# Optimization experiments

Measured on AMD Instinct MI355X. Metric: run time of the kernel, lower is better.

## Reference

```python
import jax, jax.numpy as jnp
import numpy as np

N_NODES = 100000
N_EDGES = 600000
IN_FEAT = 128
HID = 128
N_CLASSES = 64


def setup_inputs() -> dict:
    key = jax.random.key(0)
    ks = jax.random.split(key, 24)
    inp = {}
    inp["x"] = jax.random.normal(ks[0], (N_NODES, IN_FEAT), dtype=jnp.float32)
    for i, r in enumerate(["r0", "r1"]):
        inp[f"src_{r}"] = jax.random.randint(ks[1 + 3 * i], (N_EDGES,), 0, N_NODES, dtype=jnp.int32)
        inp[f"dst_{r}"] = jax.random.randint(ks[2 + 3 * i], (N_EDGES,), 0, N_NODES, dtype=jnp.int32)
        inp[f"ew_{r}"] = jax.random.uniform(ks[3 + 3 * i], (N_EDGES,), dtype=jnp.float32)
    def glorot(k, shape):
        fan = (shape[0] + shape[1]) / 2.0
        return jax.random.normal(k, shape, dtype=jnp.float32) / jnp.sqrt(fan)
    j = 7
    for r in ["r0", "r1"]:
        inp[f"Ws0_{r}"] = glorot(ks[j], (IN_FEAT, HID)); j += 1
        inp[f"Wn0_{r}"] = glorot(ks[j], (IN_FEAT, HID)); j += 1
        inp[f"b0_{r}"] = jnp.zeros((HID,), jnp.float32)
        inp[f"Wp_{r}"] = glorot(ks[j], (HID, HID)); j += 1
        inp[f"bp_{r}"] = jnp.zeros((HID,), jnp.float32)
        inp[f"Ws1_{r}"] = glorot(ks[j], (HID, N_CLASSES)); j += 1
        inp[f"Wn1_{r}"] = glorot(ks[j], (HID, N_CLASSES)); j += 1
        inp[f"b1_{r}"] = jnp.zeros((N_CLASSES,), jnp.float32)
    return inp


def _mean_agg(feat, src, dst, ew, n_nodes):
    # edge-weighted messages, mean over in-edges (divide by in-degree as DGL does)
    msg = feat[src] * ew[:, None]                      # [E, d]
    s = jax.ops.segment_sum(msg, dst, num_segments=n_nodes)
    deg = jax.ops.segment_sum(jnp.ones_like(ew), dst, num_segments=n_nodes)
    return s / jnp.maximum(deg, 1.0)[:, None]


def _max_agg(feat, src, dst, ew, n_nodes):
    msg = feat[src] * ew[:, None]                      # [E, d]
    m = jax.ops.segment_max(msg, dst, num_segments=n_nodes)
    deg = jax.ops.segment_sum(jnp.ones_like(ew), dst, num_segments=n_nodes)
    return jnp.where(deg[:, None] > 0, m, 0.0)         # zero for isolated nodes


def reference(x, src_r0, dst_r0, ew_r0, src_r1, dst_r1, ew_r1,
              Ws0_r0, Wn0_r0, b0_r0, Ws0_r1, Wn0_r1, b0_r1,
              Wp_r0, bp_r0, Ws1_r0, Wn1_r0, b1_r0,
              Wp_r1, bp_r1, Ws1_r1, Wn1_r1, b1_r1):
    n = x.shape[0]
    # Layer 0: per-relation SAGEConv(mean), HeteroGraphConv aggregate='sum', then relu
    h = jnp.zeros((n, Wn0_r0.shape[1]), x.dtype)
    for src, dst, ew, Ws, Wn, b in [
        (src_r0, dst_r0, ew_r0, Ws0_r0, Wn0_r0, b0_r0),
        (src_r1, dst_r1, ew_r1, Ws0_r1, Wn0_r1, b0_r1),
    ]:
        agg = _mean_agg(x, src, dst, ew, n)
        h = h + x @ Ws + agg @ Wn + b
    h = jax.nn.relu(h)
    # Classifier layer: per-relation SAGEConv(pool): relu(fc_pool(h_src)) -> max-agg
    logits = jnp.zeros((n, Wn1_r0.shape[1]), x.dtype)
    for src, dst, ew, Wp, bp, Ws, Wn, b in [
        (src_r0, dst_r0, ew_r0, Wp_r0, bp_r0, Ws1_r0, Wn1_r0, b1_r0),
        (src_r1, dst_r1, ew_r1, Wp_r1, bp_r1, Ws1_r1, Wn1_r1, b1_r1),
    ]:
        hp = jax.nn.relu(h @ Wp + bp)
        agg = _max_agg(hp, src, dst, ew, n)
        logits = logits + h @ Ws + agg @ Wn + b
    return logits
```

## Files before the change

### kernel.cpp

```cpp
#include <hip/hip_runtime.h>

typedef short bf16x8 __attribute__((ext_vector_type(8)));
typedef float f32x4 __attribute__((ext_vector_type(4)));
typedef float f32x2 __attribute__((ext_vector_type(2)));
typedef unsigned short u16;
typedef unsigned int u32;
typedef unsigned char u8;

#define NN 100000
#define NE 600000
#define PART 12500
#define ECH 4688

__device__ __forceinline__ u16 f2b(float f) {
    u32 u = __float_as_uint(f);
    return (u16)((u + 0x7FFFu + ((u >> 16) & 1u)) >> 16);
}

__global__ __launch_bounds__(256) void deg_part(
    const int* __restrict__ d0, const int* __restrict__ d1,
    int* __restrict__ g0, int* __restrict__ g1)
{
    int part = blockIdx.x & 7;
    int sub = blockIdx.x >> 3;
    int rel = sub & 1;
    int chunk = sub >> 1;
    const int lo = part * PART, hi = lo + PART;
    const int* d = rel ? d1 : d0;
    int* g = rel ? g1 : g0;
    const int e0 = chunk * ECH;
    const int e1 = min(e0 + ECH, NE);
    for (int e = e0 + threadIdx.x; e < e1; e += 256) {
        int dd = d[e];
        if (dd >= lo && dd < hi) atomicAdd(&g[dd], 1);
    }
}

__global__ void fused_setup(
    const float* __restrict__ x, u16* __restrict__ xo, u8* __restrict__ x8,
    const float* __restrict__ Ws0_0, const float* __restrict__ Ws0_1,
    const float* __restrict__ Wn0_0, const float* __restrict__ Wn0_1,
    const float* __restrict__ Wp_0,  const float* __restrict__ Wp_1,
    const float* __restrict__ Ws1_0, const float* __restrict__ Ws1_1,
    const float* __restrict__ Wn1_0, const float* __restrict__ Wn1_1,
    const float* __restrict__ b0_0, const float* __restrict__ b0_1,
    const float* __restrict__ b1_0, const float* __restrict__ b1_1,
    const float* __restrict__ bp_0, const float* __restrict__ bp_1,
    u16* __restrict__ w, float* __restrict__ bsum0, float* __restrict__ bsum1,
    float* __restrict__ bpc)
{
    int bb = blockIdx.x;
    if (bb < 12500) {
        int t = bb * 256 + threadIdx.x;
        const float4 v = reinterpret_cast<const float4*>(x)[t];
        ushort4 r; r.x = f2b(v.x); r.y = f2b(v.y); r.z = f2b(v.z); r.w = f2b(v.w);
        reinterpret_cast<ushort4*>(xo)[t] = r;
        u32 p = __builtin_amdgcn_cvt_pk_fp8_f32(v.x, v.y, 0, false);
        p = __builtin_amdgcn_cvt_pk_fp8_f32(v.z, v.w, p, true);
        reinterpret_cast<u32*>(x8)[t] = p;
    } else {
        int t = (bb - 12500) * 256 + threadIdx.x;
        if (t < 81920) {
            int m = t >> 14, u = t & 16383;
            int n = u >> 7, k = u & 127;
            float v;
            if (m == 0)      v = Ws0_0[k * 128 + n] + Ws0_1[k * 128 + n];
            else if (m == 1) v = Wn0_0[k * 128 + n];
            else if (m == 2) v = Wn0_1[k * 128 + n];
            else if (m == 3) v = Wp_0[k * 128 + n];
            else             v = Wp_1[k * 128 + n];
            w[t] = f2b(v);
        } else if (t < 106496) {
            int u = t - 81920;
            int m = u >> 13; u &= 8191;
            int n = u >> 7, k = u & 127;
            float v;
            if (m == 0)      v = Ws1_0[k * 64 + n] + Ws1_1[k * 64 + n];
            else if (m == 1) v = Wn1_0[k * 64 + n];
            else             v = Wn1_1[k * 64 + n];
            w[t] = f2b(v);
        } else if (t < 106624) {
            int i = t - 106496; bsum0[i] = b0_0[i] + b0_1[i];
        } else if (t < 106688) {
            int i = t - 106624; bsum1[i] = b1_0[i] + b1_1[i];
        } else if (t < 106944) {
            int i = t - 106688; bpc[i] = (i < 128) ? bp_0[i] : bp_1[i - 128];
        }
    }
}

__global__ void scan_local(const int* __restrict__ deg0, const int* __restrict__ deg1,
                           int* __restrict__ offs0, int* __restrict__ offs1,
                           int* __restrict__ bsA, int* __restrict__ bsB)
{
    __shared__ int sm[1024];
    int rel = blockIdx.x >= 98;
    int blk = blockIdx.x - rel * 98;
    const int* in = rel ? deg1 : deg0;
    int* out = rel ? offs1 : offs0;
    int* bsum = rel ? bsB : bsA;
    int t = threadIdx.x;
    int i = blk * 1024 + t;
    int v = (i < NN) ? in[i] : 0;
    sm[t] = v;
    __syncthreads();
    for (int off = 1; off < 1024; off <<= 1) {
        int add = (t >= off) ? sm[t - off] : 0;
        __syncthreads();
        sm[t] += add;
        __syncthreads();
    }
    if (i < NN) out[i] = sm[t] - v;
    if (t == 1023) bsum[blk] = sm[1023];
}

__global__ void scan_bsums(int* __restrict__ bsA, int* __restrict__ bsB)
{
    __shared__ int sm[128];
    int* bsum = blockIdx.x ? bsB : bsA;
    int t = threadIdx.x;
    int v = (t < 98) ? bsum[t] : 0;
    sm[t] = v;
    __syncthreads();
    for (int off = 1; off < 128; off <<= 1) {
        int add = (t >= off) ? sm[t - off] : 0;
        __syncthreads();
        sm[t] += add;
        __syncthreads();
    }
    if (t < 98) bsum[t] = sm[t] - v;
}

__global__ void scan_add(int* __restrict__ offs0, int* __restrict__ offs1,
                         const int* __restrict__ bsA, const int* __restrict__ bsB,
                         int* __restrict__ cur0, int* __restrict__ cur1,
                         u32* __restrict__ csr0, u32* __restrict__ csr1)
{
    int rel = blockIdx.x >= 392;
    int i = (blockIdx.x - rel * 392) * 256 + threadIdx.x;
    int* offs = rel ? offs1 : offs0;
    int* cur = rel ? cur1 : cur0;
    const int* bsum = rel ? bsB : bsA;
    if (i < NN) {
        int v = offs[i] + bsum[i >> 10];
        offs[i] = v;
        cur[i] = v;
    }
    if (i == 0) offs[NN] = NE;
    if (blockIdx.x == 0 && threadIdx.x < 8) {
        csr0[NE + threadIdx.x] = 0;
        csr1[NE + threadIdx.x] = 0;
    }
}

__global__ __launch_bounds__(256) void build_csr_part(
    const int* __restrict__ src0, const int* __restrict__ dst0,
    const float* __restrict__ ew0,
    const int* __restrict__ src1, const int* __restrict__ dst1,
    const float* __restrict__ ew1,
    int* __restrict__ cur0, int* __restrict__ cur1,
    u32* __restrict__ csr0, u32* __restrict__ csr1)
{
    int part = blockIdx.x & 7;
    int sub = blockIdx.x >> 3;
    int rel = sub & 1;
    int chunk = sub >> 1;
    const int lo = part * PART, hi = lo + PART;
    const int* src = rel ? src1 : src0;
    const int* dst = rel ? dst1 : dst0;
    const float* ew = rel ? ew1 : ew0;
    int* cur = rel ? cur1 : cur0;
    u32* csr = rel ? csr1 : csr0;
    const int e0 = chunk * ECH;
    const int e1 = min(e0 + ECH, NE);
    for (int e = e0 + threadIdx.x; e < e1; e += 256) {
        int d = dst[e];
        if (d >= lo && d < hi) {
            int p = atomicAdd(&cur[d], 1);
            u32 q = (__float_as_uint(ew[e]) + 0x10000u) >> 17;
            csr[p] = ((u32)src[e] << 15) | q;
        }
    }
}

template<bool MAXAGG, bool FP8>
__global__ __launch_bounds__(256) void gather(
    const u8* __restrict__ F0, const u8* __restrict__ F1,
    const int* __restrict__ offs0, const u32* __restrict__ csr0, u16* __restrict__ o0,
    const int* __restrict__ offs1, const u32* __restrict__ csr1, u16* __restrict__ o1)
{
    int b = blockIdx.x;
    int rel = b >= 25000;
    const u8* F = rel ? F1 : F0;
    const int* offs = rel ? offs1 : offs0;
    const u32* csr = rel ? csr1 : csr0;
    u16* out = rel ? o1 : o0;
    int node = (b - rel * 25000) * 4 + (threadIdx.x >> 6);
    int lane2 = (threadIdx.x & 63) << 1;
    int beg = __builtin_amdgcn_readfirstlane(offs[node]);
    int end = __builtin_amdgcn_readfirstlane(offs[node + 1]);

    float a0 = 0.f, a1 = 0.f;
    for (int e = beg; e < end; e += 8) {
        u32 E[8], v[8];
#pragma unroll
        for (int i = 0; i < 8; ++i)
            E[i] = csr[e + i];
#pragma unroll
        for (int i = 0; i < 8; ++i) {
            if (FP8)
                v[i] = *reinterpret_cast<const u16*>(F + ((size_t)(E[i] >> 15) << 7) + lane2);
            else
                v[i] = *reinterpret_cast<const u32*>(F + ((size_t)(E[i] >> 15) << 8) + (lane2 << 1));
        }
#pragma unroll
        for (int i = 0; i < 8; ++i) {
            float wgt = (e + i < end) ? __uint_as_float(E[i] << 17) : 0.f;
            float f0, f1;
            if (FP8) {
                f32x2 d = __builtin_amdgcn_cvt_pk_f32_fp8(v[i], false);
                f0 = d.x; f1 = d.y;
            } else {
                f0 = __uint_as_float(v[i] << 16);
                f1 = __uint_as_float(v[i] & 0xFFFF0000u);
            }
            if (MAXAGG) { a0 = fmaxf(a0, f0 * wgt); a1 = fmaxf(a1, f1 * wgt); }
            else        { a0 = fmaf(f0, wgt, a0);   a1 = fmaf(f1, wgt, a1); }
        }
    }
    float s = MAXAGG ? 1.f : 1.f / fmaxf((float)(end - beg), 1.f);
    ushort2 r; r.x = f2b(a0 * s); r.y = f2b(a1 * s);
    *reinterpret_cast<ushort2*>(out + (size_t)node * 128 + lane2) = r;
}

template<int NPAIR, int COLGROUPS, int WAVES, bool RELU, bool OUTF32, bool DUAL>
__global__ __launch_bounds__(WAVES * 64, 2) void gemm_reg(
    const u16* __restrict__ A0, const u16* __restrict__ A1, const u16* __restrict__ A2,
    const u16* __restrict__ BT, const float* __restrict__ bias,
    float* __restrict__ outF, u16* __restrict__ outB, u16* __restrict__ outB2)
{
    constexpr int NC = COLGROUPS * 32;
    constexpr int RT = WAVES / COLGROUPS;
    constexpr int OST = DUAL ? (NC / 2) : NC;
    constexpr int NTILES = NN / 32;
    const int w = threadIdx.x >> 6, l = threadIdx.x & 63;
    const int cg = w % COLGROUPS, rsub = w / COLGROUPS;
    const int l15 = l & 15, lk = (l >> 4) << 3, rq = (l >> 4) << 2;

    bf16x8 bfr[NPAIR][4][2];
#pragma unroll
    for (int p = 0; p < NPAIR; ++p)
#pragma unroll
        for (int ks = 0; ks < 4; ++ks)
#pragma unroll
            for (int cf = 0; cf < 2; ++cf) {
                int n = p * NC + cg * 32 + cf * 16 + l15;
                bfr[p][ks][cf] = *reinterpret_cast<const bf16x8*>(BT + (size_t)n * 128 + ks * 32 + lk);
            }

    const u16* As[3] = {A0, A1, A2};
    const float bv0 = bias[cg * 32 + l15];
    const float bv1 = bias[cg * 32 + 16 + l15];

    for (int tile = blockIdx.x * RT + rsub; tile < NTILES; tile += gridDim.x * RT) {
        const size_t rowbase = (size_t)tile * 32;

        bf16x8 af[NPAIR][4][2];
#pragma unroll
        for (int p = 0; p < NPAIR; ++p) {
            const u16* A = As[p] + rowbase * 128;
#pragma unroll
            for (int ks = 0; ks < 4; ++ks) {
                const int k0 = ks * 32 + lk;
                af[p][ks][0] = *reinterpret_cast<const bf16x8*>(A + (size_t)l15 * 128 + k0);
                af[p][ks][1] = *reinterpret_cast<const bf16x8*>(A + (size_t)(16 + l15) * 128 + k0);
            }
        }

        f32x4 acc[2][2];
#pragma unroll
        for (int rf = 0; rf < 2; ++rf)
#pragma unroll
            for (int cf = 0; cf < 2; ++cf)
                acc[rf][cf] = f32x4{0.f, 0.f, 0.f, 0.f};

#pragma unroll
        for (int p = 0; p < NPAIR; ++p)
#pragma unroll
            for (int ks = 0; ks < 4; ++ks) {
                acc[0][0] = __builtin_amdgcn_mfma_f32_16x16x32_bf16(af[p][ks][0], bfr[p][ks][0], acc[0][0], 0, 0, 0);
                acc[0][1] = __builtin_amdgcn_mfma_f32_16x16x32_bf16(af[p][ks][0], bfr[p][ks][1], acc[0][1], 0, 0, 0);
                acc[1][0] = __builtin_amdgcn_mfma_f32_16x16x32_bf16(af[p][ks][1], bfr[p][ks][0], acc[1][0], 0, 0, 0);
                acc[1][1] = __builtin_amdgcn_mfma_f32_16x16x32_bf16(af[p][ks][1], bfr[p][ks][1], acc[1][1], 0, 0, 0);
            }

        u16* ob = outB;
        if (DUAL && cg >= 4) ob = outB2;
        const int colbase = (DUAL ? (cg & 3) : cg) * 32;
#pragma unroll
        for (int cf = 0; cf < 2; ++cf) {
            const int col = colbase + cf * 16 + l15;
            const float bv = cf ? bv1 : bv0;
#pragma unroll
            for (int rf = 0; rf < 2; ++rf) {
#pragma unroll
                for (int j = 0; j < 4; ++j) {
                    const size_t row = rowbase + rf * 16 + rq + j;
                    float v = acc[rf][cf][j] + bv;
                    if (RELU) v = fmaxf(v, 0.f);
                    if (OUTF32) outF[row * OST + col] = v;
                    else        ob[row * OST + col] = f2b(v);
                }
            }
        }
    }
}

extern "C" void kernel_launch(void* const* d_in, const int* in_sizes, int n_in,
                              void* d_out, int out_size, void* d_ws, size_t ws_size,
                              hipStream_t stream)
{
    const float* x     = (const float*)d_in[0];
    const int*   src0  = (const int*)d_in[1];
    const int*   dst0  = (const int*)d_in[2];
    const float* ew0   = (const float*)d_in[3];
    const int*   src1  = (const int*)d_in[4];
    const int*   dst1  = (const int*)d_in[5];
    const float* ew1   = (const float*)d_in[6];
    const float* Ws0_0 = (const float*)d_in[7];
    const float* Wn0_0 = (const float*)d_in[8];
    const float* b0_0  = (const float*)d_in[9];
    const float* Wp_0  = (const float*)d_in[10];
    const float* bp_0  = (const float*)d_in[11];
    const float* Ws1_0 = (const float*)d_in[12];
    const float* Wn1_0 = (const float*)d_in[13];
    const float* b1_0  = (const float*)d_in[14];
    const float* Ws0_1 = (const float*)d_in[15];
    const float* Wn0_1 = (const float*)d_in[16];
    const float* b0_1  = (const float*)d_in[17];
    const float* Wp_1  = (const float*)d_in[18];
    const float* bp_1  = (const float*)d_in[19];
    const float* Ws1_1 = (const float*)d_in[20];
    const float* Wn1_1 = (const float*)d_in[21];
    const float* b1_1  = (const float*)d_in[22];

    char* ws = (char*)d_ws;
    u16*   x16   = (u16*)(ws + 0);
    u16*   h16   = (u16*)(ws + 25600000);
    u16*   a0    = (u16*)(ws + 51200000);
    u16*   a1    = (u16*)(ws + 76800000);
    u16*   hp1   = (u16*)(ws + 102400000);
    u32*   csr0  = (u32*)(ws + 128000000);
    u32*   csr1  = (u32*)(ws + 130400032);
    int*   offs0 = (int*)(ws + 132800064);
    int*   offs1 = (int*)(ws + 133200080);
    int*   cur0  = (int*)(ws + 133600096);
    int*   cur1  = (int*)(ws + 134000096);
    int*   deg0  = (int*)(ws + 134400096);
    int*   deg1  = (int*)(ws + 134800096);
    int*   bsA   = (int*)(ws + 135200096);
    int*   bsB   = (int*)(ws + 135200608);
    u16*   wts   = (u16*)(ws + 135201120);
    float* bsum0 = (float*)(ws + 135414112);
    float* bsum1 = (float*)(ws + 135414624);
    float* bpc   = (float*)(ws + 135415136);
    u8*    x8    = (u8*)(ws + 136000000);

    u16* hp0 = x16;

    hipMemsetAsync(deg0, 0, 800000, stream);
    deg_part<<<2048, 256, 0, stream>>>(dst0, dst1, deg0, deg1);
    fused_setup<<<12918, 256, 0, stream>>>(
        x, x16, x8, Ws0_0, Ws0_1, Wn0_0, Wn0_1, Wp_0, Wp_1,
        Ws1_0, Ws1_1, Wn1_0, Wn1_1, b0_0, b0_1, b1_0, b1_1, bp_0, bp_1,
        wts, bsum0, bsum1, bpc);

    scan_local<<<196, 1024, 0, stream>>>(deg0, deg1, offs0, offs1, bsA, bsB);
    scan_bsums<<<2, 128, 0, stream>>>(bsA, bsB);
    scan_add<<<784, 256, 0, stream>>>(offs0, offs1, bsA, bsB, cur0, cur1, csr0, csr1);
    build_csr_part<<<2048, 256, 0, stream>>>(
        src0, dst0, ew0, src1, dst1, ew1, cur0, cur1, csr0, csr1);

    gather<false, true><<<50000, 256, 0, stream>>>(
        x8, x8, offs0, csr0, a0, offs1, csr1, a1);
    gemm_reg<3, 4, 4, true, false, false><<<1024, 256, 0, stream>>>(
        x16, a0, a1, wts, bsum0, nullptr, h16, nullptr);

    gemm_reg<1, 8, 8, true, false, true><<<512, 512, 0, stream>>>(
        h16, nullptr, nullptr, wts + 49152, bpc, nullptr, hp0, hp1);
    gather<true, false><<<50000, 256, 0, stream>>>(
        (const u8*)hp0, (const u8*)hp1, offs0, csr0, a0, offs1, csr1, a1);
    gemm_reg<3, 2, 4, false, true, false><<<782, 256, 0, stream>>>(
        h16, a0, a1, wts + 81920, bsum1, (float*)d_out, nullptr, nullptr);
}
```

Measured before the change: 362.3 us.

## Stage A tiles through swizzled double-buffered LDS in first two GEMMs

Adds a gemm_lds kernel that loads each 32-row A tile once into LDS with an XOR swizzle, double-buffers it, and prefetches the next tile into registers while MFMAs run on the current one. It replaces gemm_reg for the layer-0 GEMM and the pool-projection GEMM, with grid sizes changed to 768 persistent blocks. The aim is to stop waves sharing a tile from each re-reading A from global memory and to hide load latency. In exchange it adds LDS usage, a barrier per tile, and drops the occupancy hint from launch_bounds.

```diff
diff --git a/kernel.cpp b/kernel.cpp
--- a/kernel.cpp
+++ b/kernel.cpp
@@ -233,6 +233,129 @@
     *reinterpret_cast<ushort2*>(out + (size_t)node * 128 + lane2) = r;
 }
 
+template<int NPAIR, int COLGROUPS, int WAVES, bool RELU, bool DUAL>
+__global__ __launch_bounds__(WAVES * 64) void gemm_lds(
+    const u16* __restrict__ A0, const u16* __restrict__ A1, const u16* __restrict__ A2,
+    const u16* __restrict__ BT, const float* __restrict__ bias,
+    u16* __restrict__ outB, u16* __restrict__ outB2)
+{
+    constexpr int NC = COLGROUPS * 32;
+    constexpr int OST = DUAL ? (NC / 2) : NC;
+    constexpr int NTILES = NN / 32;
+    constexpr int THREADS = WAVES * 64;
+    constexpr int NLOAD = NPAIR * 512 / THREADS;
+    __shared__ char lds[2 * NPAIR * 8192];
+
+    const int t = threadIdx.x;
+    const int w = t >> 6, l = t & 63;
+    const int cg = w % COLGROUPS;
+    const int l15 = l & 15, lk = (l >> 4) << 3, rq = (l >> 4) << 2;
+
+    const u16* As[3] = {A0, A1, A2};
+
+    int goff[NLOAD], loff[NLOAD];
+#pragma unroll
+    for (int j = 0; j < NLOAD; ++j) {
+        const int p = (j * THREADS) >> 9;
+        const int s = ((j * THREADS) & 511) + t;
+        goff[j] = s * 8;
+        loff[j] = p * 8192 + ((s * 16) ^ (((s >> 4) & 7) << 4));
+    }
+
+    bf16x8 bfr[NPAIR][4][2];
+#pragma unroll
+    for (int p = 0; p < NPAIR; ++p)
+#pragma unroll
+        for (int ks = 0; ks < 4; ++ks)
+#pragma unroll
+            for (int cf = 0; cf < 2; ++cf) {
+                int n = p * NC + cg * 32 + cf * 16 + l15;
+                bfr[p][ks][cf] = *reinterpret_cast<const bf16x8*>(BT + (size_t)n * 128 + ks * 32 + lk);
+            }
+    const float bv0 = bias[cg * 32 + l15];
+    const float bv1 = bias[cg * 32 + 16 + l15];
+
+    u16* ob = outB;
+    if (DUAL && cg >= 4) ob = outB2;
+    const int colbase = (DUAL ? (cg & 3) : cg) * 32;
+
+    uint4 v[NLOAD];
+    int tile = blockIdx.x;
+#pragma unroll
+    for (int j = 0; j < NLOAD; ++j) {
+        const int p = (j * THREADS) >> 9;
+        v[j] = *reinterpret_cast<const uint4*>(As[p] + (size_t)tile * 4096 + goff[j]);
+    }
+#pragma unroll
+    for (int j = 0; j < NLOAD; ++j)
+        *reinterpret_cast<uint4*>(&lds[loff[j]]) = v[j];
+    __syncthreads();
+
+    int buf = 0;
+    while (tile < NTILES) {
+        const int nxt = tile + (int)gridDim.x;
+        if (nxt < NTILES) {
+#pragma unroll
+            for (int j = 0; j < NLOAD; ++j) {
+                const int p = (j * THREADS) >> 9;
+                v[j] = *reinterpret_cast<const uint4*>(As[p] + (size_t)nxt * 4096 + goff[j]);
+            }
+        }
+
+        const int bb = buf * NPAIR * 8192;
+        f32x4 acc[2][2];
+#pragma unroll
+        for (int rf = 0; rf < 2; ++rf)
+#pragma unroll
+            for (int cf = 0; cf < 2; ++cf)
+                acc[rf][cf] = f32x4{0.f, 0.f, 0.f, 0.f};
+        const int sw = (l15 & 7) << 4;
+#pragma unroll
+        for (int p = 0; p < NPAIR; ++p) {
+            const int base = bb + p * 8192;
+#pragma unroll
+            for (int ks = 0; ks < 4; ++ks) {
+                const int cbyte = ks * 64 + lk * 2;
+                bf16x8 a0 = *reinterpret_cast<const bf16x8*>(
+                    &lds[base + ((l15 * 256 + cbyte) ^ sw)]);
+                bf16x8 a1 = *reinterpret_cast<const bf16x8*>(
+                    &lds[base + (((16 + l15) * 256 + cbyte) ^ sw)]);
+                acc[0][0] = __builtin_amdgcn_mfma_f32_16x16x32_bf16(a0, bfr[p][ks][0], acc[0][0], 0, 0, 0);
+                acc[0][1] = __builtin_amdgcn_mfma_f32_16x16x32_bf16(a0, bfr[p][ks][1], acc[0][1], 0, 0, 0);
+                acc[1][0] = __builtin_amdgcn_mfma_f32_16x16x32_bf16(a1, bfr[p][ks][0], acc[1][0], 0, 0, 0);
+                acc[1][1] = __builtin_amdgcn_mfma_f32_16x16x32_bf16(a1, bfr[p][ks][1], acc[1][1], 0, 0, 0);
+            }
+        }
+
+        const size_t rowbase = (size_t)tile * 32;
+#pragma unroll
+        for (int cf = 0; cf < 2; ++cf) {
+            const int col = colbase + cf * 16 + l15;
+            const float bv = cf ? bv1 : bv0;
+#pragma unroll
+            for (int rf = 0; rf < 2; ++rf) {
+#pragma unroll
+                for (int j = 0; j < 4; ++j) {
+                    const size_t row = rowbase + rf * 16 + rq + j;
+                    float vv = acc[rf][cf][j] + bv;
+                    if (RELU) vv = fmaxf(vv, 0.f);
+                    ob[row * OST + col] = f2b(vv);
+                }
+            }
+        }
+
+        if (nxt < NTILES) {
+            const int ob2 = (buf ^ 1) * NPAIR * 8192;
+#pragma unroll
+            for (int j = 0; j < NLOAD; ++j)
+                *reinterpret_cast<uint4*>(&lds[ob2 + loff[j]]) = v[j];
+        }
+        __syncthreads();
+        buf ^= 1;
+        tile = nxt;
+    }
+}
+
 template<int NPAIR, int COLGROUPS, int WAVES, bool RELU, bool OUTF32, bool DUAL>
 __global__ __launch_bounds__(WAVES * 64, 2) void gemm_reg(
     const u16* __restrict__ A0, const u16* __restrict__ A1, const u16* __restrict__ A2,
@@ -383,11 +506,11 @@
 
     gather<false, true><<<50000, 256, 0, stream>>>(
         x8, x8, offs0, csr0, a0, offs1, csr1, a1);
-    gemm_reg<3, 4, 4, true, false, false><<<1024, 256, 0, stream>>>(
-        x16, a0, a1, wts, bsum0, nullptr, h16, nullptr);
-
-    gemm_reg<1, 8, 8, true, false, true><<<512, 512, 0, stream>>>(
-        h16, nullptr, nullptr, wts + 49152, bpc, nullptr, hp0, hp1);
+    gemm_lds<3, 4, 4, true, false><<<768, 256, 0, stream>>>(
+        x16, a0, a1, wts, bsum0, h16, nullptr);
+
+    gemm_lds<1, 8, 8, true, true><<<768, 512, 0, stream>>>(
+        h16, nullptr, nullptr, wts + 49152, bpc, hp0, hp1);
     gather<true, false><<<50000, 256, 0, stream>>>(
         (const u8*)hp0, (const u8*)hp1, offs0, csr0, a0, offs1, csr1, a1);
     gemm_reg<3, 2, 4, false, true, false><<<782, 256, 0, stream>>>(
```

After: 328.2 us. 1.1x faster.
